# Optimization experiments

Measured on AMD Instinct MI355X. Metric: run time of the kernel, lower is better.

The kernel has to match this reference:

```python
import jax, jax.numpy as jnp
import numpy as np
from math import factorial

LMAX = 3
NMAX = 3
RC = 6.0
UNIT = RC / 6.0  # atomic_unit
NSPEC = 4        # numbers take values 0..3 (static species set)
L = LMAX + 1


def _nnl():
    a = np.array([[1.0 / ((2 * l + 1) * 2 ** (2 * n + l) * factorial(n) * factorial(n + l))
                   for l in range(L)] for n in range(NMAX + 1)])
    return jnp.asarray(np.sqrt(a[None] * a[:, None]), jnp.float32)  # (nmax+1, nmax+1, L)


def _yr_yi():
    one = np.ones((L, L))
    Yr = 2 * np.tril(one) - np.eye(L)   # real-part weights (m=0 on diag -> weight 1)
    Yi = 2 * np.triu(one, 1)            # imag-part weights (m>=1)
    return jnp.asarray(Yr, jnp.float32), jnp.asarray(Yi, jnp.float32)


def _ylm(xyz):
    """Regular solid harmonics R_l^m (FMM normalization) on the (L,L) grid:
    grid[l, l-m] = Re R_l^m, grid[l-m, l] = Im R_l^m (m>=1). Returns (L, L, N)."""
    x, y, z = xyz[:, 0], xyz[:, 1], xyz[:, 2]
    r2 = x * x + y * y + z * z
    Re = {(0, 0): jnp.ones_like(x)}
    Im = {(0, 0): jnp.zeros_like(x)}
    for l in range(1, L):
        # R_l^l = (x + i y) / (2l) * R_{l-1}^{l-1}
        Re[(l, l)] = (x * Re[(l - 1, l - 1)] - y * Im[(l - 1, l - 1)]) / (2 * l)
        Im[(l, l)] = (x * Im[(l - 1, l - 1)] + y * Re[(l - 1, l - 1)]) / (2 * l)
        # R_l^{l-1} = z * R_{l-1}^{l-1}
        Re[(l, l - 1)] = z * Re[(l - 1, l - 1)]
        Im[(l, l - 1)] = z * Im[(l - 1, l - 1)]
        for m in range(0, l - 1):
            den = (l + m) * (l - m)
            Re[(l, m)] = ((2 * l - 1) * z * Re[(l - 1, m)] - r2 * Re[(l - 2, m)]) / den
            Im[(l, m)] = ((2 * l - 1) * z * Im[(l - 1, m)] - r2 * Im[(l - 2, m)]) / den
    Y = jnp.zeros((L, L) + x.shape, dtype=xyz.dtype)
    for l in range(L):
        for m in range(l + 1):
            Y = Y.at[l, l - m].set(Re[(l, m)])
            if m >= 1:
                Y = Y.at[l - m, l].set(Im[(l, m)])
    return Y


def reference(coo, numbers):
    xyz = coo / UNIT
    d = jnp.sqrt(jnp.sum(xyz * xyz, axis=-1))            # (N,)
    D = UNIT * d
    cutoff = jnp.where(D < RC, (1.0 - D / RC) ** 2, 0.0)  # polynomial radial cutoff
    r = jnp.exp(-0.5 * D ** 2 / UNIT ** 2) * cutoff       # Exp(-0.5 I^2/unit^2)*radial
    n = 2.0 * jnp.arange(NMAX + 1, dtype=coo.dtype)       # (nmax+1,)
    f = r[None] * d[None] ** n[:, None]                   # (nmax+1, N)
    Y = _ylm(xyz)                                         # (L, L, N)
    ff = f[:, None, None] * Y[None]                       # (nmax+1, L, L, N)
    # species-grouped segmented reduction (replaces per-species index_select + sum)
    c = jax.ops.segment_sum(jnp.moveaxis(ff, -1, 0), numbers.astype(jnp.int32),
                            num_segments=NSPEC)           # (S, nmax+1, L, L)
    nnp = c[None, :, None] * c[:, None, :, None]          # (S, S, n+1, n+1, L, L)
    Yr, Yi = _yr_yi()
    p = (nnp * Yr).sum(axis=-1) + (nnp * Yi).sum(axis=-2)  # (S, S, n+1, n+1, L)
    p = p * _nnl()
    p = p / (jnp.linalg.norm(p) + jnp.finfo(p.dtype).eps)
    return p.reshape(NSPEC * NSPEC, -1)                   # (S^2, (n+1)^2*L) dense COO values


def setup_inputs() -> dict:
    key = jax.random.key(0)
    k1, k2 = jax.random.split(key)
    N = 1_000_000
    coo = 3.0 * jax.random.normal(k1, (N, 3), dtype=jnp.float32)
    numbers = jax.random.randint(k2, (N,), 0, NSPEC)
    return {"coo": coo, "numbers": numbers}
```

## Files before the change

kernel.cpp:

```cpp
#include <hip/hip_runtime.h>
#include <math.h>

constexpr int   BT   = 256;
constexpr int   TILE = 1024;
constexpr int   CAP  = 160;
constexpr int   NREP = 8;
constexpr float RC   = 6.0f;

__device__ inline void global_fadd(float* p, float v) {
    unsafeAtomicAdd(p, v);
}

__global__ __launch_bounds__(256) void soap_zero(float* __restrict__ c) {
    c[blockIdx.x * 256 + threadIdx.x] = 0.0f;
}

__device__ __forceinline__ void soap_atom(float* acc, float x, float y, float z,
                                          float f0) {
    const float r2 = x * x + y * y + z * z;
    const float f1 = f0 * r2;
    const float f2 = f1 * r2;
    const float f3 = f2 * r2;

    #define ACC4(q, val) do { const float yv_ = (val);          \
        acc[(q)]      = fmaf(f0, yv_, acc[(q)]);                \
        acc[16 + (q)] = fmaf(f1, yv_, acc[16 + (q)]);           \
        acc[32 + (q)] = fmaf(f2, yv_, acc[32 + (q)]);           \
        acc[48 + (q)] = fmaf(f3, yv_, acc[48 + (q)]); } while (0)

    acc[0] += f0; acc[16] += f1; acc[32] += f2; acc[48] += f3;
    const float Re11 = 0.5f * x, Im11 = 0.5f * y, Re10 = z;
    ACC4(5, Re10); ACC4(4, Re11); ACC4(1, Im11);
    const float Re22 = 0.25f * (x * Re11 - y * Im11);
    const float Im22 = 0.25f * (x * Im11 + y * Re11);
    const float Re21 = z * Re11, Im21 = z * Im11;
    const float Re20 = 0.25f * (3.0f * z * Re10 - r2);
    ACC4(10, Re20); ACC4(9, Re21); ACC4(6, Im21); ACC4(8, Re22); ACC4(2, Im22);
    const float Re33 = (x * Re22 - y * Im22) * (1.0f / 6.0f);
    const float Im33 = (x * Im22 + y * Re22) * (1.0f / 6.0f);
    const float Re32 = z * Re22, Im32 = z * Im22;
    const float Re30 = (5.0f * z * Re20 - r2 * Re10) * (1.0f / 9.0f);
    const float Re31 = (5.0f * z * Re21 - r2 * Re11) * (1.0f / 8.0f);
    const float Im31 = (5.0f * z * Im21 - r2 * Im11) * (1.0f / 8.0f);
    ACC4(15, Re30); ACC4(14, Re31); ACC4(11, Im31); ACC4(13, Re32);
    ACC4(7, Im32); ACC4(12, Re33); ACC4(3, Im33);
    #undef ACC4
}

__device__ __forceinline__ float soap_radial(float x, float y, float z) {
    const float r2 = x * x + y * y + z * z;
    const float dd = sqrtf(r2);
    const float t  = fmaxf(1.0f - dd * (1.0f / RC), 0.0f);
    return __expf(-0.5f * r2) * t * t;
}

__global__ __launch_bounds__(BT, 3) void soap_accum(const float* __restrict__ coo,
                                                    const int*   __restrict__ numbers,
                                                    float*       __restrict__ c_glob,
                                                    int n) {
    __shared__ float4 bins[4][4][CAP];
    __shared__ int    cnts[4][4];
    __shared__ unsigned long long ovf[4][4];

    const int lane = threadIdx.x & 63;
    const int w    = threadIdx.x >> 6;
    const int nb4  = n >> 2;

    const float4* __restrict__ coo4 = (const float4*)coo;
    const int4*   __restrict__ num4 = (const int4*)numbers;

    const int q  = (blockIdx.x * TILE >> 2) + threadIdx.x;
    const int jq = (q < nb4) ? q : (nb4 - 1);
    const float4 A = coo4[3 * jq + 0];
    const float4 B = coo4[3 * jq + 1];
    const float4 C = coo4[3 * jq + 2];
    const int4   S = num4[jq];
    const bool   qv = (q < nb4);

    const float ax[4] = {A.x, A.w, B.z, C.y};
    const float ay[4] = {A.y, B.x, B.w, C.z};
    const float az[4] = {A.z, B.y, C.x, C.w};
    const int   as[4] = {S.x, S.y, S.z, S.w};

    int cur0 = 0, cur1 = 0, cur2 = 0, cur3 = 0;
    const unsigned long long below = (1ull << lane) - 1ull;
    #pragma unroll
    for (int slot = 0; slot < 4; ++slot) {
        unsigned long long ov = 0;
        #pragma unroll
        for (int sp = 0; sp < 4; ++sp) {
            int& cur = (sp == 0) ? cur0 : (sp == 1) ? cur1 : (sp == 2) ? cur2 : cur3;
            const bool m = qv && (as[slot] == sp);
            const unsigned long long bal = __ballot(m);
            const int pos = cur + __popcll(bal & below);
            if (m && pos < CAP)
                bins[w][sp][pos] = make_float4(ax[slot], ay[slot], az[slot], 0.0f);
            ov |= __ballot(m && pos >= CAP);
            cur += __popcll(bal);
        }
        if (lane == 0) ovf[w][slot] = ov;
    }
    if (lane == 0) {
        cnts[w][0] = (cur0 < CAP) ? cur0 : CAP;
        cnts[w][1] = (cur1 < CAP) ? cur1 : CAP;
        cnts[w][2] = (cur2 < CAP) ? cur2 : CAP;
        cnts[w][3] = (cur3 < CAP) ? cur3 : CAP;
    }
    __syncthreads();

    float acc[64];
    #pragma unroll
    for (int k = 0; k < 64; ++k) acc[k] = 0.0f;

    #pragma unroll
    for (int seg = 0; seg < 4; ++seg) {
        const int c = cnts[seg][w];
        #pragma unroll 1
        for (int base = 0; base < c; base += 64) {
            const int  idx   = base + lane;
            const int  ridx  = (idx < CAP) ? idx : (CAP - 1);
            const float4 v   = bins[seg][w][ridx];
            const bool valid = (idx < c);
            const float vx = valid ? v.x : 0.0f;
            const float vy = valid ? v.y : 0.0f;
            const float vz = valid ? v.z : 0.0f;
            const float f0 = valid ? soap_radial(vx, vy, vz) : 0.0f;
            soap_atom(acc, vx, vy, vz, f0);
        }
    }

    unsigned long long anyov = 0;
    #pragma unroll
    for (int w2 = 0; w2 < 4; ++w2)
        #pragma unroll
        for (int slot = 0; slot < 4; ++slot) anyov |= ovf[w2][slot];
    if (anyov != 0ull) {
        for (int w2 = 0; w2 < 4; ++w2)
            for (int slot = 0; slot < 4; ++slot) {
                unsigned long long m = ovf[w2][slot];
                while (m != 0ull) {
                    const int b = __builtin_ctzll(m);
                    m &= m - 1ull;
                    const int atom = 4 * ((blockIdx.x * TILE >> 2) + w2 * 64 + b) + slot;
                    const float x = coo[3 * atom + 0];
                    const float y = coo[3 * atom + 1];
                    const float z = coo[3 * atom + 2];
                    const int   s = numbers[atom];
                    const bool  use = (s == w && lane == 0);
                    const float xx = use ? x : 0.0f;
                    const float yy = use ? y : 0.0f;
                    const float zz = use ? z : 0.0f;
                    const float f0 = use ? soap_radial(xx, yy, zz) : 0.0f;
                    soap_atom(acc, xx, yy, zz, f0);
                }
            }
    }

    #pragma unroll
    for (int m = 32; m >= 1; m >>= 1) {
        const bool hi = (lane & m) != 0;
        #pragma unroll
        for (int qq = 0; qq < m; ++qq) {
            const float give = hi ? acc[qq] : acc[qq + m];
            const float keep = hi ? acc[qq + m] : acc[qq];
            acc[qq] = keep + __shfl_xor(give, m, 64);
        }
    }
    global_fadd(&c_glob[(blockIdx.x & (NREP - 1)) * 256 + w * 64 + lane], acc[0]);
}

__global__ __launch_bounds__(1024) void soap_finish(const float* __restrict__ c_glob,
                                                    float* __restrict__ out) {
    __shared__ float c[256];
    __shared__ float red[16];
    __shared__ float snorm;
    const int t = threadIdx.x;
    if (t < 256) {
        float s = 0.0f;
        #pragma unroll
        for (int rep = 0; rep < NREP; ++rep) s += c_glob[rep * 256 + t];
        c[t] = s;
    }
    __syncthreads();

    const int x  = t & 3;
    const int nn = (t >> 2) & 3;
    const int kk = (t >> 4) & 3;
    const int j  = (t >> 6) & 3;
    const int i  = (t >> 8) & 3;

    float p1 = 0.0f, p2 = 0.0f;
    #pragma unroll
    for (int b = 0; b < 4; ++b) {
        const float yr = (x > b) ? 2.0f : ((x == b) ? 1.0f : 0.0f);
        p1 += yr * c[((j * 4 + nn) * 4 + x) * 4 + b] * c[((i * 4 + kk) * 4 + x) * 4 + b];
    }
    #pragma unroll
    for (int a = 0; a < 4; ++a) {
        const float yi = (x > a) ? 2.0f : 0.0f;
        p2 += yi * c[((j * 4 + nn) * 4 + a) * 4 + x] * c[((i * 4 + kk) * 4 + a) * 4 + x];
    }

    const double fact[8] = {1, 1, 2, 6, 24, 120, 720, 5040};
    const double ak = 1.0 / ((2 * x + 1) * exp2((double)(2 * kk + x)) * fact[kk] * fact[kk + x]);
    const double an = 1.0 / ((2 * x + 1) * exp2((double)(2 * nn + x)) * fact[nn] * fact[nn + x]);
    const float val = (p1 + p2) * (float)sqrt(ak * an);

    float sq = val * val;
    #pragma unroll
    for (int off = 32; off > 0; off >>= 1) sq += __shfl_down(sq, off, 64);
    if ((t & 63) == 0) red[t >> 6] = sq;
    __syncthreads();
    if (t == 0) {
        float ssum = 0.0f;
        #pragma unroll
        for (int ww = 0; ww < 16; ++ww) ssum += red[ww];
        snorm = sqrtf(ssum);
    }
    __syncthreads();

    out[t] = val / (snorm + 1.1920929e-07f);
}

extern "C" void kernel_launch(void* const* d_in, const int* in_sizes, int n_in,
                              void* d_out, int out_size, void* d_ws, size_t ws_size,
                              hipStream_t stream) {
    const float* coo     = (const float*)d_in[0];
    const int*   numbers = (const int*)d_in[1];
    const int    n       = in_sizes[1];
    float*       c_glob  = (float*)d_ws;
    float*       out     = (float*)d_out;

    const int nblocks = (n + TILE - 1) / TILE;

    soap_zero  <<<NREP,    256, 0, stream>>>(c_glob);
    soap_accum <<<nblocks, BT,  0, stream>>>(coo, numbers, c_glob, n);
    soap_finish<<<1,      1024, 0, stream>>>(c_glob, out);
}
```

Baseline: 78.86 us.

## Fuse finish stage into accumulation kernel via last-block counter

```diff
diff --git a/kernel.cpp b/kernel.cpp
--- a/kernel.cpp
+++ b/kernel.cpp
@@ -9,10 +9,6 @@
 
 __device__ inline void global_fadd(float* p, float v) {
     unsafeAtomicAdd(p, v);
-}
-
-__global__ __launch_bounds__(256) void soap_zero(float* __restrict__ c) {
-    c[blockIdx.x * 256 + threadIdx.x] = 0.0f;
 }
 
 __device__ __forceinline__ void soap_atom(float* acc, float x, float y, float z,
@@ -54,10 +50,12 @@
     return __expf(-0.5f * r2) * t * t;
 }
 
-__global__ __launch_bounds__(BT, 3) void soap_accum(const float* __restrict__ coo,
+__global__ __launch_bounds__(BT, 3) void soap_fused(const float* __restrict__ coo,
                                                     const int*   __restrict__ numbers,
                                                     float*       __restrict__ c_glob,
-                                                    int n) {
+                                                    int*         __restrict__ counter,
+                                                    float*       __restrict__ out,
+                                                    int n, int nblocks) {
     __shared__ float4 bins[4][4][CAP];
     __shared__ int    cnts[4][4];
     __shared__ unsigned long long ovf[4][4];
@@ -167,18 +165,27 @@
         }
     }
     global_fadd(&c_glob[(blockIdx.x & (NREP - 1)) * 256 + w * 64 + lane], acc[0]);
-}
-
-__global__ __launch_bounds__(1024) void soap_finish(const float* __restrict__ c_glob,
-                                                    float* __restrict__ out) {
+
+    __shared__ int is_last;
+    __threadfence();
+    if (threadIdx.x == 0) {
+        const int old = __hip_atomic_fetch_add(counter, 1, __ATOMIC_ACQ_REL,
+                                               __HIP_MEMORY_SCOPE_AGENT);
+        is_last = (old == nblocks - 1);
+    }
+    __syncthreads();
+    if (!is_last) return;
+
     __shared__ float c[256];
-    __shared__ float red[16];
+    __shared__ float red[4];
     __shared__ float snorm;
     const int t = threadIdx.x;
-    if (t < 256) {
+    {
         float s = 0.0f;
         #pragma unroll
-        for (int rep = 0; rep < NREP; ++rep) s += c_glob[rep * 256 + t];
+        for (int rep = 0; rep < NREP; ++rep)
+            s += __hip_atomic_load(&c_glob[rep * 256 + t], __ATOMIC_RELAXED,
+                                   __HIP_MEMORY_SCOPE_AGENT);
         c[t] = s;
     }
     __syncthreads();
@@ -187,39 +194,43 @@
     const int nn = (t >> 2) & 3;
     const int kk = (t >> 4) & 3;
     const int j  = (t >> 6) & 3;
-    const int i  = (t >> 8) & 3;
-
-    float p1 = 0.0f, p2 = 0.0f;
-    #pragma unroll
-    for (int b = 0; b < 4; ++b) {
-        const float yr = (x > b) ? 2.0f : ((x == b) ? 1.0f : 0.0f);
-        p1 += yr * c[((j * 4 + nn) * 4 + x) * 4 + b] * c[((i * 4 + kk) * 4 + x) * 4 + b];
-    }
-    #pragma unroll
-    for (int a = 0; a < 4; ++a) {
-        const float yi = (x > a) ? 2.0f : 0.0f;
-        p2 += yi * c[((j * 4 + nn) * 4 + a) * 4 + x] * c[((i * 4 + kk) * 4 + a) * 4 + x];
-    }
 
     const double fact[8] = {1, 1, 2, 6, 24, 120, 720, 5040};
     const double ak = 1.0 / ((2 * x + 1) * exp2((double)(2 * kk + x)) * fact[kk] * fact[kk + x]);
     const double an = 1.0 / ((2 * x + 1) * exp2((double)(2 * nn + x)) * fact[nn] * fact[nn + x]);
-    const float val = (p1 + p2) * (float)sqrt(ak * an);
-
-    float sq = val * val;
+    const float nnl = (float)sqrt(ak * an);
+
+    float val0, val1, val2, val3, sq = 0.0f;
+    #define DO_I(i, dst) do {                                                    \
+        float p1 = 0.0f, p2 = 0.0f;                                              \
+        _Pragma("unroll")                                                        \
+        for (int b = 0; b < 4; ++b) {                                            \
+            const float yr = (x > b) ? 2.0f : ((x == b) ? 1.0f : 0.0f);          \
+            p1 += yr * c[((j * 4 + nn) * 4 + x) * 4 + b]                         \
+                     * c[(((i) * 4 + kk) * 4 + x) * 4 + b];                      \
+        }                                                                        \
+        _Pragma("unroll")                                                        \
+        for (int a = 0; a < 4; ++a) {                                            \
+            const float yi = (x > a) ? 2.0f : 0.0f;                              \
+            p2 += yi * c[((j * 4 + nn) * 4 + a) * 4 + x]                         \
+                     * c[(((i) * 4 + kk) * 4 + a) * 4 + x];                      \
+        }                                                                        \
+        dst = (p1 + p2) * nnl;  sq = fmaf(dst, dst, sq); } while (0)
+    DO_I(0, val0); DO_I(1, val1); DO_I(2, val2); DO_I(3, val3);
+    #undef DO_I
+
     #pragma unroll
     for (int off = 32; off > 0; off >>= 1) sq += __shfl_down(sq, off, 64);
-    if ((t & 63) == 0) red[t >> 6] = sq;
-    __syncthreads();
-    if (t == 0) {
-        float ssum = 0.0f;
-        #pragma unroll
-        for (int ww = 0; ww < 16; ++ww) ssum += red[ww];
-        snorm = sqrtf(ssum);
-    }
-    __syncthreads();
-
-    out[t] = val / (snorm + 1.1920929e-07f);
+    if (lane == 0) red[w] = sq;
+    __syncthreads();
+    if (t == 0) snorm = sqrtf(red[0] + red[1] + red[2] + red[3]);
+    __syncthreads();
+
+    const float inv = 1.0f / (snorm + 1.1920929e-07f);
+    out[0 * 256 + t] = val0 * inv;
+    out[1 * 256 + t] = val1 * inv;
+    out[2 * 256 + t] = val2 * inv;
+    out[3 * 256 + t] = val3 * inv;
 }
 
 extern "C" void kernel_launch(void* const* d_in, const int* in_sizes, int n_in,
@@ -229,11 +240,11 @@
     const int*   numbers = (const int*)d_in[1];
     const int    n       = in_sizes[1];
     float*       c_glob  = (float*)d_ws;
+    int*         counter = (int*)((char*)d_ws + NREP * 256 * sizeof(float));
     float*       out     = (float*)d_out;
 
     const int nblocks = (n + TILE - 1) / TILE;
 
-    soap_zero  <<<NREP,    256, 0, stream>>>(c_glob);
-    soap_accum <<<nblocks, BT,  0, stream>>>(coo, numbers, c_glob, n);
-    soap_finish<<<1,      1024, 0, stream>>>(c_glob, out);
-}
+    hipMemsetAsync(d_ws, 0, NREP * 256 * sizeof(float) + sizeof(int), stream);
+    soap_fused<<<nblocks, BT, 0, stream>>>(coo, numbers, c_glob, counter, out, n, nblocks);
+}
```

New measurement: 143.4 us. 1.82x slower.
